# Performance work log

Measured on AMD Instinct MI355X. Metric: run time of the kernel, lower is better.

The kernel has to match this reference:

```python
import jax, jax.numpy as jnp
import numpy as np

B, L, H, E = 8, 1024, 8, 64
S, D = 1024, 64


def fp(x):
    # power-norm with p=2: norm(x) * x^2 / norm(x^2)
    norm = jnp.sqrt(jnp.sum(x * x, axis=-1, keepdims=True))
    px = x * x  # x^p, p=2
    pnorm = jnp.sqrt(jnp.sum(px * px, axis=-1, keepdims=True))
    return norm * px / pnorm


def phi_p(x):
    return fp(jax.nn.relu(x))


def setup_inputs() -> dict:
    key = jax.random.key(0)
    kq, kk, kv = jax.random.split(key, 3)
    queries = jax.random.normal(kq, (B, L, H, E), dtype=jnp.float32)
    keys = jax.random.normal(kk, (B, S, H, E), dtype=jnp.float32)
    values = jax.random.normal(kv, (B, S, H, D), dtype=jnp.float32)
    # all-False mask: masked_fill(-inf) + fp() would NaN otherwise (see notes)
    attn_mask = jnp.zeros((B, 1, L, S), dtype=bool)
    return {"queries": queries, "keys": keys, "values": values, "attn_mask": attn_mask}


def reference(queries, keys, values, attn_mask):
    qt = phi_p(queries)              # [B,L,H,E]
    kt = phi_p(keys)                 # [B,S,H,E]
    scores = jnp.einsum('blhe,bshe->bhls', qt, kt)  # [B,H,L,S]
    scores = jnp.where(attn_mask, -jnp.inf, scores)  # mask_flag=True path
    # NB: original computes scale = 1/sqrt(E) but never applies it.
    A = jax.nn.softmax(fp(scores), axis=-1)  # dropout is identity at eval
    V = jnp.einsum('bhls,bshd->blhd', A, values)  # [B,L,H,D]
    return V
```

## Files before the change

### kernel.cpp

```cpp
#include <hip/hip_runtime.h>
#include <hip/hip_bf16.h>


#define B_ 8
#define L_ 1024
#define H_ 8
#define E_ 64
#define S_ 1024
#define D_ 64
#define BH_ 64

typedef _Float16 f16_t;
typedef _Float16 f16x8 __attribute__((ext_vector_type(8)));
typedef _Float16 f16x4v __attribute__((ext_vector_type(4)));
typedef float f32x4 __attribute__((ext_vector_type(4)));

#define MFMA16F(a, b, c) __builtin_amdgcn_mfma_f32_16x16x32_f16(a, b, c, 0, 0, 0)
#define GLDS16(g, l)                                                        \
  __builtin_amdgcn_global_load_lds(                                         \
      (const __attribute__((address_space(1))) void*)(g),                   \
      (__attribute__((address_space(3))) void*)(l), 16, 0, 0)

#if __has_builtin(__builtin_amdgcn_exp2f)
#define EXP2(x) __builtin_amdgcn_exp2f(x)
#else
#define EXP2(x) exp2f(x)
#endif

__global__ __launch_bounds__(256) void prep_kernel(
    const float* __restrict__ q, const float* __restrict__ k,
    const float* __restrict__ v, f16_t* __restrict__ qf,
    f16_t* __restrict__ kf, f16_t* __restrict__ vt) {
  __shared__ float tile[32][68];
  int bid = blockIdx.x;
  if (bid < 8192) {
    int row = bid * 16 + (threadIdx.x >> 4);
    int p = threadIdx.x & 15;
    const float* src;
    f16_t* dst;
    int r = row;
    if (r < B_ * L_ * H_) { src = q; dst = qf; }
    else { r -= B_ * L_ * H_; src = k; dst = kf; }
    int b = r >> 13;
    int l = (r >> 3) & 1023;
    int h = r & 7;
    float4 x = ((const float4*)(src + (size_t)r * 64))[p];
    float s0 = fmaxf(x.x, 0.f) * fmaxf(x.x, 0.f);
    float s1 = fmaxf(x.y, 0.f) * fmaxf(x.y, 0.f);
    float s2 = fmaxf(x.z, 0.f) * fmaxf(x.z, 0.f);
    float s3 = fmaxf(x.w, 0.f) * fmaxf(x.w, 0.f);
    float sum2 = (s0 + s1) + (s2 + s3);
    float sum4 = fmaf(s0, s0, s1 * s1) + fmaf(s2, s2, s3 * s3);
#pragma unroll
    for (int off = 1; off < 16; off <<= 1) {
      sum2 += __shfl_xor(sum2, off, 64);
      sum4 += __shfl_xor(sum4, off, 64);
    }
    float sc = (sum4 > 0.f) ? sqrtf(sum2 / sum4) : 0.f;
    f16x4v o = {(f16_t)(sc * s0), (f16_t)(sc * s1), (f16_t)(sc * s2),
                (f16_t)(sc * s3)};
    int c = p >> 1, e = (p & 1) * 4;
    int col = (((c ^ (l & 7)) << 3) | e);
    *(f16x4v*)(dst + ((size_t)(b * H_ + h) * 1024 + l) * 64 + col) = o;
  } else {
    int vb = bid - 8192;
    int bh = vb >> 5;
    int st = vb & 31;
    int b = bh >> 3, h = bh & 7;
    int t = threadIdx.x;
    int sl = t >> 3, dp = t & 7;
    const float* src =
        v + (((size_t)(b * S_ + st * 32 + sl) * H_ + h) * D_) + dp * 8;
    float4 f0 = ((const float4*)src)[0];
    float4 f1 = ((const float4*)src)[1];
    *(float4*)&tile[sl][dp * 8] = f0;
    *(float4*)&tile[sl][dp * 8 + 4] = f1;
    __syncthreads();
    int d = t >> 2, sc = t & 3;
    f16_t tmp[8];
#pragma unroll
    for (int j = 0; j < 8; ++j) tmp[j] = (f16_t)tile[sc * 8 + j][d];
    f16_t* dst = vt + (((size_t)bh * 32 + st) * 64 + d) * 32 + sc * 8;
    *(uint4*)dst = *(const uint4*)tmp;
  }
}

__global__ __launch_bounds__(256, 4) void attn_kernel(
    const f16_t* __restrict__ qf, const f16_t* __restrict__ kf,
    const f16_t* __restrict__ vt, float* __restrict__ out) {
  __shared__ __align__(16) f16_t k_t[2][2048];
  __shared__ __align__(16) f16_t v_t[2][2048];
  __shared__ __align__(16) f16_t wbuf[4][16 * 40];

  int bh = blockIdx.x & 63;
  int qb = blockIdx.x >> 6;
  int b = bh >> 3, h = bh & 7;
  int tid = threadIdx.x;
  int wave = tid >> 6, lane = tid & 63;
  int g = lane >> 4, n = lane & 15;

  const f16_t* qf_b = qf + ((size_t)bh * L_ + qb * 64) * 64;
  const f16_t* kf_b = kf + (size_t)bh * S_ * 64;
  const f16_t* vt_b = vt + (size_t)bh * 32 * 2048;

  int arow = wave * 16 + n;
  int qoff = arow * 64 + ((g ^ (n & 7)) << 3);
  f16x8 qa0 = *(const f16x8*)(qf_b + qoff);
  f16x8 qa1 = *(const f16x8*)(qf_b + (qoff ^ 32));

  int koff = n * 64 + ((g ^ (n & 7)) << 3);
  int lds_o = tid * 8;

  const f32x4 fzero = {0.f, 0.f, 0.f, 0.f};
  f32x4 acc2 = fzero, acc4 = fzero, mx = fzero;

  const f16_t* kg = kf_b;
#pragma unroll 2
  for (int t = 0; t < 32; ++t) {
    f16x8 b00 = *(const f16x8*)(kg + koff);
    f16x8 b01 = *(const f16x8*)(kg + (koff ^ 32));
    f16x8 b10 = *(const f16x8*)(kg + koff + 1024);
    f16x8 b11 = *(const f16x8*)(kg + (koff ^ 32) + 1024);
    kg += 2048;
    f32x4 sc0 = MFMA16F(qa0, b00, fzero);
    sc0 = MFMA16F(qa1, b01, sc0);
    f32x4 sc1 = MFMA16F(qa0, b10, fzero);
    sc1 = MFMA16F(qa1, b11, sc1);
    f32x4 t0 = sc0 * sc0, t1 = sc1 * sc1;
    acc2 += t0 + t1;
    acc4 += t0 * t0;
    acc4 += t1 * t1;
    mx = __builtin_elementwise_max(mx, __builtin_elementwise_max(t0, t1));
  }
  float a2[4], a4[4], m2[4];
#pragma unroll
  for (int r = 0; r < 4; ++r) { a2[r] = acc2[r]; a4[r] = acc4[r]; m2[r] = mx[r]; }
#pragma unroll
  for (int off = 1; off < 16; off <<= 1)
#pragma unroll
    for (int r = 0; r < 4; ++r) {
      a2[r] += __shfl_xor(a2[r], off, 64);
      a4[r] += __shfl_xor(a4[r], off, 64);
      m2[r] = fmaxf(m2[r], __shfl_xor(m2[r], off, 64));
    }
  const float LOG2E = 1.44269504f;
  f32x4 c2v, cm2v;
#pragma unroll
  for (int r = 0; r < 4; ++r) {
    float cr = (a4[r] > 0.f) ? (sqrtf(a2[r] / a4[r]) * LOG2E) : 0.f;
    c2v[r] = cr;
    cm2v[r] = cr * m2[r];
  }

  f32x4 pv[4];
#pragma unroll
  for (int dg = 0; dg < 4; ++dg) pv[dg] = fzero;
  f32x4 denv = fzero;
  f16_t* wb = wbuf[wave];

  GLDS16(kf_b + lds_o, &k_t[0][lds_o]);
  GLDS16(vt_b + lds_o, &v_t[0][lds_o]);
  for (int t = 0; t < 32; ++t) {
    __syncthreads();
    if (t < 31) {
      int go = (t + 1) * 2048 + lds_o;
      int bs = (t + 1) & 1;
      GLDS16(kf_b + go, &k_t[bs][lds_o]);
      GLDS16(vt_b + go, &v_t[bs][lds_o]);
    }
    const f16_t* kt = k_t[t & 1];
    const f16_t* vl = v_t[t & 1];
    f16x8 vb[4];
#pragma unroll
    for (int dg = 0; dg < 4; ++dg)
      vb[dg] = *(const f16x8*)(vl + n * 32 + dg * 512 + g * 8);
    f16x8 b00 = *(const f16x8*)(kt + koff);
    f16x8 b01 = *(const f16x8*)(kt + (koff ^ 32));
    f16x8 b10 = *(const f16x8*)(kt + koff + 1024);
    f16x8 b11 = *(const f16x8*)(kt + (koff ^ 32) + 1024);
    f32x4 sc0 = MFMA16F(qa0, b00, fzero);
    sc0 = MFMA16F(qa1, b01, sc0);
    f32x4 sc1 = MFMA16F(qa0, b10, fzero);
    sc1 = MFMA16F(qa1, b11, sc1);
    f32x4 e0 = sc0 * sc0 * c2v - cm2v;
    f32x4 e1 = sc1 * sc1 * c2v - cm2v;
    f32x4 w0, w1;
#pragma unroll
    for (int r = 0; r < 4; ++r) { w0[r] = EXP2(e0[r]); w1[r] = EXP2(e1[r]); }
    denv += w0 + w1;
#pragma unroll
    for (int r = 0; r < 4; ++r) {
      wb[(g * 4 + r) * 40 + n] = (f16_t)w0[r];
      wb[(g * 4 + r) * 40 + 16 + n] = (f16_t)w1[r];
    }
    f16x8 wa = *(const f16x8*)(wb + n * 40 + g * 8);
#pragma unroll
    for (int dg = 0; dg < 4; ++dg) pv[dg] = MFMA16F(wa, vb[dg], pv[dg]);
  }
  float den[4];
#pragma unroll
  for (int r = 0; r < 4; ++r) den[r] = denv[r];
#pragma unroll
  for (int off = 1; off < 16; off <<= 1)
#pragma unroll
    for (int r = 0; r < 4; ++r) den[r] += __shfl_xor(den[r], off, 64);
#pragma unroll
  for (int r = 0; r < 4; ++r) {
    float inv = 1.f / den[r];
    int l = qb * 64 + wave * 16 + g * 4 + r;
    float* op = out + (((size_t)b * L_ + l) * H_ + h) * D_;
#pragma unroll
    for (int dg = 0; dg < 4; ++dg) op[dg * 16 + n] = pv[dg][r] * inv;
  }
}

extern "C" void kernel_launch(void* const* d_in, const int* in_sizes, int n_in,
                              void* d_out, int out_size, void* d_ws, size_t ws_size,
                              hipStream_t stream) {
  const float* q = (const float*)d_in[0];
  const float* k = (const float*)d_in[1];
  const float* v = (const float*)d_in[2];
  float* out = (float*)d_out;

  const size_t NE = (size_t)B_ * L_ * H_ * E_;
  f16_t* qf = (f16_t*)d_ws;
  f16_t* kf = qf + NE;
  f16_t* vt = kf + NE;

  prep_kernel<<<8192 + 2048, 256, 0, stream>>>(q, k, v, qf, kf, vt);
  attn_kernel<<<BH_ * (L_ / 64), 256, 0, stream>>>(qf, kf, vt, out);
}
```

Baseline: 162.6 us.

## Transpose score MFMA and pack softmax weights via permlane swaps instead of LDS

Swaps the operand order of the QK^T MFMAs so each lane holds scores for a single query row. This lets the row statistics be reduced with two cross-group shuffles instead of a four-step shuffle tree per register. The softmax weights are packed to f16 pairs and rearranged into the PV MFMA A-operand layout with permlane32/16 swaps, which removes the per-wave LDS round trip through wbuf. The risk is that the permlane builtins may be unavailable and fall back to shuffles, and the register remapping must match the MFMA layout exactly.

```diff
diff --git a/kernel.cpp b/kernel.cpp
--- a/kernel.cpp
+++ b/kernel.cpp
@@ -14,6 +14,7 @@
 typedef _Float16 f16x8 __attribute__((ext_vector_type(8)));
 typedef _Float16 f16x4v __attribute__((ext_vector_type(4)));
 typedef float f32x4 __attribute__((ext_vector_type(4)));
+typedef unsigned u32x4 __attribute__((ext_vector_type(4)));
 
 #define MFMA16F(a, b, c) __builtin_amdgcn_mfma_f32_16x16x32_f16(a, b, c, 0, 0, 0)
 #define GLDS16(g, l)                                                        \
@@ -26,6 +27,40 @@
 #else
 #define EXP2(x) exp2f(x)
 #endif
+
+static __device__ __forceinline__ unsigned pkh(float a, float b) {
+  return __builtin_bit_cast(unsigned, __builtin_amdgcn_cvt_pkrtz(a, b));
+}
+
+static __device__ __forceinline__ void pl32_swap(unsigned& x, unsigned& y) {
+#if __has_builtin(__builtin_amdgcn_permlane32_swap)
+  auto r = __builtin_amdgcn_permlane32_swap(x, y, false, false);
+  x = r[0];
+  y = r[1];
+#else
+  unsigned xs = __shfl_xor((int)x, 32, 64), ys = __shfl_xor((int)y, 32, 64);
+  bool hi = (threadIdx.x & 32) != 0;
+  unsigned nx = hi ? ys : x;
+  unsigned ny = hi ? y : xs;
+  x = nx;
+  y = ny;
+#endif
+}
+
+static __device__ __forceinline__ void pl16_swap(unsigned& x, unsigned& y) {
+#if __has_builtin(__builtin_amdgcn_permlane16_swap)
+  auto r = __builtin_amdgcn_permlane16_swap(x, y, false, false);
+  x = r[0];
+  y = r[1];
+#else
+  unsigned xs = __shfl_xor((int)x, 16, 64), ys = __shfl_xor((int)y, 16, 64);
+  bool odd = (threadIdx.x & 16) != 0;
+  unsigned nx = odd ? ys : x;
+  unsigned ny = odd ? y : xs;
+  x = nx;
+  y = ny;
+#endif
+}
 
 __global__ __launch_bounds__(256) void prep_kernel(
     const float* __restrict__ q, const float* __restrict__ k,
@@ -90,7 +125,6 @@
     const f16_t* __restrict__ vt, float* __restrict__ out) {
   __shared__ __align__(16) f16_t k_t[2][2048];
   __shared__ __align__(16) f16_t v_t[2][2048];
-  __shared__ __align__(16) f16_t wbuf[4][16 * 40];
 
   int bh = blockIdx.x & 63;
   int qb = blockIdx.x >> 6;
@@ -122,41 +156,33 @@
     f16x8 b10 = *(const f16x8*)(kg + koff + 1024);
     f16x8 b11 = *(const f16x8*)(kg + (koff ^ 32) + 1024);
     kg += 2048;
-    f32x4 sc0 = MFMA16F(qa0, b00, fzero);
-    sc0 = MFMA16F(qa1, b01, sc0);
-    f32x4 sc1 = MFMA16F(qa0, b10, fzero);
-    sc1 = MFMA16F(qa1, b11, sc1);
+    f32x4 sc0 = MFMA16F(b00, qa0, fzero);
+    sc0 = MFMA16F(b01, qa1, sc0);
+    f32x4 sc1 = MFMA16F(b10, qa0, fzero);
+    sc1 = MFMA16F(b11, qa1, sc1);
     f32x4 t0 = sc0 * sc0, t1 = sc1 * sc1;
     acc2 += t0 + t1;
     acc4 += t0 * t0;
     acc4 += t1 * t1;
     mx = __builtin_elementwise_max(mx, __builtin_elementwise_max(t0, t1));
   }
-  float a2[4], a4[4], m2[4];
-#pragma unroll
-  for (int r = 0; r < 4; ++r) { a2[r] = acc2[r]; a4[r] = acc4[r]; m2[r] = mx[r]; }
-#pragma unroll
-  for (int off = 1; off < 16; off <<= 1)
-#pragma unroll
-    for (int r = 0; r < 4; ++r) {
-      a2[r] += __shfl_xor(a2[r], off, 64);
-      a4[r] += __shfl_xor(a4[r], off, 64);
-      m2[r] = fmaxf(m2[r], __shfl_xor(m2[r], off, 64));
-    }
+  float a2 = (acc2[0] + acc2[1]) + (acc2[2] + acc2[3]);
+  float a4 = (acc4[0] + acc4[1]) + (acc4[2] + acc4[3]);
+  float m2 = fmaxf(fmaxf(mx[0], mx[1]), fmaxf(mx[2], mx[3]));
+  a2 += __shfl_xor(a2, 16, 64);
+  a4 += __shfl_xor(a4, 16, 64);
+  m2 = fmaxf(m2, __shfl_xor(m2, 16, 64));
+  a2 += __shfl_xor(a2, 32, 64);
+  a4 += __shfl_xor(a4, 32, 64);
+  m2 = fmaxf(m2, __shfl_xor(m2, 32, 64));
   const float LOG2E = 1.44269504f;
-  f32x4 c2v, cm2v;
-#pragma unroll
-  for (int r = 0; r < 4; ++r) {
-    float cr = (a4[r] > 0.f) ? (sqrtf(a2[r] / a4[r]) * LOG2E) : 0.f;
-    c2v[r] = cr;
-    cm2v[r] = cr * m2[r];
-  }
+  float c2 = (a4 > 0.f) ? (sqrtf(a2 / a4) * LOG2E) : 0.f;
+  float cm2 = c2 * m2;
 
   f32x4 pv[4];
 #pragma unroll
   for (int dg = 0; dg < 4; ++dg) pv[dg] = fzero;
   f32x4 denv = fzero;
-  f16_t* wb = wbuf[wave];
 
   GLDS16(kf_b + lds_o, &k_t[0][lds_o]);
   GLDS16(vt_b + lds_o, &v_t[0][lds_o]);
@@ -178,35 +204,34 @@
     f16x8 b01 = *(const f16x8*)(kt + (koff ^ 32));
     f16x8 b10 = *(const f16x8*)(kt + koff + 1024);
     f16x8 b11 = *(const f16x8*)(kt + (koff ^ 32) + 1024);
-    f32x4 sc0 = MFMA16F(qa0, b00, fzero);
-    sc0 = MFMA16F(qa1, b01, sc0);
-    f32x4 sc1 = MFMA16F(qa0, b10, fzero);
-    sc1 = MFMA16F(qa1, b11, sc1);
-    f32x4 e0 = sc0 * sc0 * c2v - cm2v;
-    f32x4 e1 = sc1 * sc1 * c2v - cm2v;
+    f32x4 sc0 = MFMA16F(b00, qa0, fzero);
+    sc0 = MFMA16F(b01, qa1, sc0);
+    f32x4 sc1 = MFMA16F(b10, qa0, fzero);
+    sc1 = MFMA16F(b11, qa1, sc1);
+    f32x4 e0 = sc0 * sc0 * c2 - cm2;
+    f32x4 e1 = sc1 * sc1 * c2 - cm2;
     f32x4 w0, w1;
 #pragma unroll
     for (int r = 0; r < 4; ++r) { w0[r] = EXP2(e0[r]); w1[r] = EXP2(e1[r]); }
     denv += w0 + w1;
-#pragma unroll
-    for (int r = 0; r < 4; ++r) {
-      wb[(g * 4 + r) * 40 + n] = (f16_t)w0[r];
-      wb[(g * 4 + r) * 40 + 16 + n] = (f16_t)w1[r];
-    }
-    f16x8 wa = *(const f16x8*)(wb + n * 40 + g * 8);
+    unsigned X0 = pkh(w0[0], w0[1]), X1 = pkh(w0[2], w0[3]);
+    unsigned Y0 = pkh(w1[0], w1[1]), Y1 = pkh(w1[2], w1[3]);
+    pl32_swap(X0, Y0);
+    pl16_swap(X0, Y0);
+    pl32_swap(X1, Y1);
+    pl16_swap(X1, Y1);
+    u32x4 fu = {X0, X1, Y0, Y1};
+    f16x8 wa = __builtin_bit_cast(f16x8, fu);
 #pragma unroll
     for (int dg = 0; dg < 4; ++dg) pv[dg] = MFMA16F(wa, vb[dg], pv[dg]);
   }
-  float den[4];
-#pragma unroll
-  for (int r = 0; r < 4; ++r) den[r] = denv[r];
-#pragma unroll
-  for (int off = 1; off < 16; off <<= 1)
-#pragma unroll
-    for (int r = 0; r < 4; ++r) den[r] += __shfl_xor(den[r], off, 64);
+  float den = (denv[0] + denv[1]) + (denv[2] + denv[3]);
+  den += __shfl_xor(den, 16, 64);
+  den += __shfl_xor(den, 32, 64);
 #pragma unroll
   for (int r = 0; r < 4; ++r) {
-    float inv = 1.f / den[r];
+    float dr = __shfl(den, g * 4 + r, 64);
+    float inv = 1.f / dr;
     int l = qb * 64 + wave * 16 + g * 4 + r;
     float* op = out + (((size_t)b * L_ + l) * H_ + h) * D_;
 #pragma unroll
```

Result: faster. 157.3 us (-3.2%).
